# Optimization experiments

Hardware: AMD Instinct MI355X
Metric: run time of the kernel (lower is better)

## Reference

```python
import jax, jax.numpy as jnp
import numpy as np

D_MODEL = 1024
HIDDEN = 2048
D_STATE = 16
KERN = 3
BATCH = 2
SEQ = 2048


def _layernorm(x, g, b, eps=1e-5):
    m = jnp.mean(x, axis=-1, keepdims=True)
    v = jnp.var(x, axis=-1, keepdims=True)
    return (x - m) * jax.lax.rsqrt(v + eps) * g + b


def setup_inputs() -> dict:
    key = jax.random.key(0)
    ks = jax.random.split(key, 10)
    w_scale = 0.02  # keep pre-activations in a sane range (mimics trained-net init)
    return {
        "x": jax.random.normal(ks[0], (BATCH, SEQ, D_MODEL), jnp.float32),
        "W_x": jax.random.normal(ks[1], (HIDDEN, D_MODEL), jnp.float32) * w_scale,
        "b_x": jnp.zeros((HIDDEN,), jnp.float32),
        "W_g": jax.random.normal(ks[2], (HIDDEN, D_MODEL), jnp.float32) * w_scale,
        "b_g": jnp.zeros((HIDDEN,), jnp.float32),
        "conv_w": jax.random.normal(ks[3], (HIDDEN, 1, KERN), jnp.float32) * 0.3,
        "conv_b": jnp.zeros((HIDDEN,), jnp.float32),
        "A_raw": jax.random.normal(ks[4], (HIDDEN, D_STATE), jnp.float32),
        "B_ssm": jax.random.normal(ks[5], (HIDDEN, D_STATE), jnp.float32),
        "C_ssm": jax.random.normal(ks[6], (HIDDEN, D_STATE), jnp.float32),
        "W_dt": jax.random.normal(ks[7], (HIDDEN, D_MODEL), jnp.float32) * w_scale,
        "b_dt": jnp.zeros((HIDDEN,), jnp.float32),
        "W_out": jax.random.normal(ks[8], (D_MODEL, HIDDEN), jnp.float32) * w_scale,
        "b_out": jnp.zeros((D_MODEL,), jnp.float32),
        "ln_g": jnp.ones((D_MODEL,), jnp.float32),
        "ln_b": jnp.zeros((D_MODEL,), jnp.float32),
    }


def reference(x, W_x, b_x, W_g, b_g, conv_w, conv_b, A_raw, B_ssm, C_ssm,
              W_dt, b_dt, W_out, b_out, ln_g, ln_b):
    # projections: u, gate
    u = jnp.einsum('bld,hd->blh', x, W_x) + b_x                    # [B,L,H]
    g = jax.nn.sigmoid(jnp.einsum('bld,hd->blh', x, W_g) + b_g)    # [B,L,H]
    # depthwise conv over time (padding = kernel//2, 'same' for odd kernel)
    pad = conv_w.shape[-1] // 2
    h = jax.lax.conv_general_dilated(
        jnp.transpose(u, (0, 2, 1)), conv_w,
        window_strides=(1,), padding=[(pad, pad)],
        feature_group_count=conv_w.shape[0],
        dimension_numbers=('NCH', 'OIH', 'NCH')) + conv_b[None, :, None]
    h = jnp.transpose(h, (0, 2, 1))                                # [B,L,H]
    u = u * g + h * (1.0 - g)
    # time-invariant dt per channel (mean over batch & time, clamped)
    dt = jax.nn.softplus(jnp.einsum('bld,hd->blh', x, W_dt) + b_dt).mean(axis=(0, 1))
    dt = jnp.clip(dt, 1e-3, 2.0)                                   # [H]
    # discretize
    A = -jax.nn.softplus(A_raw)                                    # [H,S]
    A_d = jnp.exp(A * dt[:, None])                                 # [H,S]
    B_d = (A_d - 1.0) / (A + 1e-6) * B_ssm                         # [H,S]
    # selective scan: state s[b,h,k] = A_d*s + B_d*u_t ; y = <s, C>
    Bsz, L, H = u.shape
    S = A_d.shape[1]

    def step(carry, u_t):                                          # u_t: [B,H]
        new = A_d[None] * carry + B_d[None] * u_t[:, :, None]      # [B,H,S]
        y_t = jnp.einsum('bhs,hs->bh', new, C_ssm)
        return new, y_t

    init = jnp.zeros((Bsz, H, S), dtype=u.dtype)
    _, ys = jax.lax.scan(step, init, jnp.transpose(u, (1, 0, 2)))  # ys: [L,B,H]
    y = jnp.transpose(ys, (1, 0, 2))                               # [B,L,H]
    out = jnp.einsum('blh,dh->bld', y, W_out) + b_out
    return _layernorm(x + out, ln_g, ln_b)
```

## Files before the change

### kernel.cpp

```cpp
#include <hip/hip_runtime.h>
#include <math.h>

#define D_MODEL 1024
#define HIDDEN  2048
#define D_STATE 16
#define BATCH   2
#define SEQ     2048
#define NTOK    (BATCH*SEQ)
#define CHUNK   64
#define NCHUNK  (SEQ/CHUNK)

typedef __attribute__((ext_vector_type(8))) short bf16x8;
typedef __attribute__((ext_vector_type(8))) unsigned short ushort8;
typedef __attribute__((ext_vector_type(4))) float f32x4;

#define GLOAD_LDS16(gptr, lptr) \
    __builtin_amdgcn_global_load_lds((const __attribute__((address_space(1))) void*)(gptr), \
                                     (__attribute__((address_space(3))) void*)(lptr), 16, 0, 0)

__device__ __forceinline__ float softplus_f(float x) {
    return fmaxf(x, 0.0f) + log1pf(expf(-fabsf(x)));
}
__device__ __forceinline__ float sigmoid_f(float x) {
    return 1.0f / (1.0f + expf(-x));
}
__device__ __forceinline__ ushort f2bf(float f) {
    unsigned u = __float_as_uint(f);
    unsigned r = (u + 0x7fffu + ((u >> 16) & 1u)) >> 16;
    return (ushort)r;
}
__device__ __forceinline__ float bf2f(ushort u) {
    return __uint_as_float(((unsigned)u) << 16);
}

__global__ __launch_bounds__(256) void cvt_all(
    const float* __restrict__ x, const float* __restrict__ Wx,
    const float* __restrict__ Wg, const float* __restrict__ Wdt,
    const float* __restrict__ Wout, ushort* __restrict__ arena)
{
    int i = blockIdx.x * 256 + threadIdx.x;
    const float* src; int base;
    if      (i < 1048576) { src = x;    base = 0; }
    else if (i < 1572864) { src = Wx;   base = 1048576; }
    else if (i < 2097152) { src = Wg;   base = 1572864; }
    else if (i < 2621440) { src = Wdt;  base = 2097152; }
    else                  { src = Wout; base = 2621440; }
    float4 v = reinterpret_cast<const float4*>(src)[i - base];
    ushort4 o = { f2bf(v.x), f2bf(v.y), f2bf(v.z), f2bf(v.w) };
    reinterpret_cast<ushort4*>(arena)[i] = o;
}

__device__ __forceinline__ void kloop_pipe1024(
    const ushort* __restrict__ A, const ushort* __restrict__ B,
    int ldA, int ldB, ushort* As, ushort* Bs,
    f32x4 (&acc)[4][4], int lane, int w, int wm, int wn)
{
    const int lr   = lane >> 2;
    const int kc   = (lane & 3) * 8;
    const int quad = lane >> 4;
    const int fr   = lane & 15;

    const int slab0 = w * 2;
    const int r0 = slab0 * 16 + lr;
    const int r1 = r0 + 16;
    const ushort* pa0 = A + (size_t)r0 * ldA + kc;
    const ushort* pa1 = A + (size_t)r1 * ldA + kc;
    const ushort* pb0 = B + (size_t)r0 * ldB + kc;
    const ushort* pb1 = B + (size_t)r1 * ldB + kc;

    GLOAD_LDS16(pa0,      &As[slab0 * 512]);
    GLOAD_LDS16(pa1,      &As[slab0 * 512 + 512]);
    GLOAD_LDS16(pb0,      &Bs[slab0 * 512]);
    GLOAD_LDS16(pb1,      &Bs[slab0 * 512 + 512]);
    GLOAD_LDS16(pa0 + 32, &As[4096 + slab0 * 512]);
    GLOAD_LDS16(pa1 + 32, &As[4096 + slab0 * 512 + 512]);
    GLOAD_LDS16(pb0 + 32, &Bs[4096 + slab0 * 512]);
    GLOAD_LDS16(pb1 + 32, &Bs[4096 + slab0 * 512 + 512]);

    #pragma unroll
    for (int i = 0; i < 32; i++) {
        if (i == 31) { asm volatile("s_waitcnt vmcnt(0) lgkmcnt(0)" ::: "memory"); }
        else         { asm volatile("s_waitcnt vmcnt(4) lgkmcnt(0)" ::: "memory"); }
        asm volatile("s_barrier" ::: "memory");
        if (i + 2 < 32) {
            const int nb = (i + 2) % 3;
            GLOAD_LDS16(pa0 + (i + 2) * 32, &As[nb * 4096 + slab0 * 512]);
            GLOAD_LDS16(pa1 + (i + 2) * 32, &As[nb * 4096 + slab0 * 512 + 512]);
            GLOAD_LDS16(pb0 + (i + 2) * 32, &Bs[nb * 4096 + slab0 * 512]);
            GLOAD_LDS16(pb1 + (i + 2) * 32, &Bs[nb * 4096 + slab0 * 512 + 512]);
        }
        const int buf = i % 3;
        const ushort* as = &As[buf * 4096];
        const ushort* bs = &Bs[buf * 4096];
        bf16x8 af[4], bfv[4];
        #pragma unroll
        for (int t = 0; t < 4; t++) {
            af[t]  = *reinterpret_cast<const bf16x8*>(&as[(wm * 64 + t * 16 + fr) * 32 + quad * 8]);
            bfv[t] = *reinterpret_cast<const bf16x8*>(&bs[(wn * 64 + t * 16 + fr) * 32 + quad * 8]);
        }
        #pragma unroll
        for (int ii = 0; ii < 4; ii++)
            #pragma unroll
            for (int jj = 0; jj < 4; jj++)
                acc[ii][jj] = __builtin_amdgcn_mfma_f32_16x16x32_bf16(af[ii], bfv[jj], acc[ii][jj], 0, 0, 0);
    }
    asm volatile("s_waitcnt vmcnt(0) lgkmcnt(0)" ::: "memory");
    asm volatile("s_barrier" ::: "memory");
}

__global__ __launch_bounds__(256) void proj_gemm_fused(
    const ushort* __restrict__ xbf, const ushort* __restrict__ Wcat,
    const float* __restrict__ b_x, const float* __restrict__ b_g,
    const float* __restrict__ b_dt, ushort* __restrict__ u_out,
    ushort* __restrict__ g_out, float* __restrict__ dt_sum)
{
    __shared__ ushort S[24576];
    ushort* As = S;
    ushort* Bs = S + 12288;
    const int tid = threadIdx.x, lane = tid & 63, w = tid >> 6;
    const int wm = w & 1, wn = w >> 1;
    const int m0 = blockIdx.x * 128, n0 = blockIdx.y * 128;
    const int quad = lane >> 4, fr = lane & 15;

    f32x4 acc[4][4];
    #pragma unroll
    for (int i = 0; i < 4; i++)
        #pragma unroll
        for (int j = 0; j < 4; j++)
            acc[i][j] = (f32x4){0.f, 0.f, 0.f, 0.f};

    kloop_pipe1024(xbf + (size_t)m0 * D_MODEL, Wcat + (size_t)n0 * D_MODEL,
                   D_MODEL, D_MODEL, As, Bs, acc, lane, w, wm, wn);

    const int region = n0 >> 11;
    const int ncb = n0 & 2047;

    if (region == 2) {
        #pragma unroll
        for (int j = 0; j < 4; j++) {
            int n = ncb + wn * 64 + j * 16 + fr;
            float bj = b_dt[n];
            float s = 0.f;
            #pragma unroll
            for (int i = 0; i < 4; i++)
                #pragma unroll
                for (int r = 0; r < 4; r++)
                    s += softplus_f(acc[i][j][r] + bj);
            s += __shfl_xor(s, 16);
            s += __shfl_xor(s, 32);
            if (lane < 16) atomicAdd(&dt_sum[n], s);
        }
    } else {
        const float* bias = region ? b_g : b_x;
        ushort* out = region ? g_out : u_out;
        ushort* Cs = S;
        #pragma unroll
        for (int j = 0; j < 4; j++) {
            int col = wn * 64 + j * 16 + fr;
            float bj = bias[ncb + col];
            #pragma unroll
            for (int i = 0; i < 4; i++) {
                int row = wm * 64 + i * 16 + quad * 4;
                #pragma unroll
                for (int r = 0; r < 4; r++) {
                    float v = acc[i][j][r] + bj;
                    if (region) v = sigmoid_f(v);
                    Cs[(row + r) * 128 + col] = f2bf(v);
                }
            }
        }
        __syncthreads();
        #pragma unroll
        for (int k = 0; k < 8; k++) {
            int v = k * 256 + tid;
            int row = v >> 4, c = (v & 15) * 8;
            *reinterpret_cast<ushort8*>(&out[(size_t)(m0 + row) * HIDDEN + ncb + c]) =
                *reinterpret_cast<const ushort8*>(&Cs[v * 8]);
        }
    }
}

__global__ __launch_bounds__(256) void gemm_out(
    const ushort* __restrict__ ybf, const ushort* __restrict__ Wout,
    float* __restrict__ p0, float* __restrict__ p1)
{
    __shared__ ushort S[24576];
    ushort* As = S;
    ushort* Bs = S + 12288;
    const int tid = threadIdx.x, lane = tid & 63, w = tid >> 6;
    const int wm = w & 1, wn = w >> 1;
    const int m0 = blockIdx.x * 128;
    const int nt = blockIdx.y >> 1, ks = blockIdx.y & 1;
    const int n0 = nt * 128;
    const int quad = lane >> 4, fr = lane & 15;

    f32x4 acc[4][4];
    #pragma unroll
    for (int i = 0; i < 4; i++)
        #pragma unroll
        for (int j = 0; j < 4; j++)
            acc[i][j] = (f32x4){0.f, 0.f, 0.f, 0.f};

    kloop_pipe1024(ybf + (size_t)m0 * HIDDEN + ks * 1024,
                   Wout + (size_t)n0 * HIDDEN + ks * 1024,
                   HIDDEN, HIDDEN, As, Bs, acc, lane, w, wm, wn);

    float* pk = ks ? p1 : p0;
    float* Sf = (float*)S;
    #pragma unroll
    for (int phase = 0; phase < 2; phase++) {
        if (wm == phase) {
            #pragma unroll
            for (int j = 0; j < 4; j++) {
                int col = wn * 64 + j * 16 + fr;
                #pragma unroll
                for (int i = 0; i < 4; i++) {
                    int row = i * 16 + quad * 4;
                    #pragma unroll
                    for (int r = 0; r < 4; r++)
                        Sf[(row + r) * 128 + col] = acc[i][j][r];
                }
            }
        }
        __syncthreads();
        #pragma unroll
        for (int k = 0; k < 8; k++) {
            int v = k * 256 + tid;
            int row = v >> 5, c = (v & 31) * 4;
            size_t off = (size_t)(m0 + phase * 64 + row) * D_MODEL + n0 + c;
            *reinterpret_cast<float4*>(&pk[off]) =
                *reinterpret_cast<const float4*>(&Sf[v * 4]);
        }
        __syncthreads();
    }
}

__global__ __launch_bounds__(256) void dt_finalize(
    const float* __restrict__ dt_sum, const float* __restrict__ A_raw,
    const float* __restrict__ B_ssm, float* __restrict__ A_d,
    float* __restrict__ B_d, float* __restrict__ A_dL)
{
    int i = blockIdx.x * 256 + threadIdx.x;
    if (i >= HIDDEN * D_STATE) return;
    int h = i >> 4;
    float dt = dt_sum[h] * (1.0f / NTOK);
    dt = fminf(fmaxf(dt, 1e-3f), 2.0f);
    float Av = -softplus_f(A_raw[i]);
    float Ad = expf(Av * dt);
    float Bd = (Ad - 1.0f) / (Av + 1e-6f) * B_ssm[i];
    A_d[i] = Ad;
    B_d[i] = Bd;
    A_dL[i] = expf(Av * dt * CHUNK);
}

__global__ __launch_bounds__(256) void scan_pass1(
    const ushort* __restrict__ u_bf, const ushort* __restrict__ g_bf,
    const float* __restrict__ conv_w, const float* __restrict__ conv_b,
    const float* __restrict__ A_d, const float* __restrict__ B_d,
    const float* __restrict__ C_ssm,
    ushort* __restrict__ ypart, float* __restrict__ states)
{
    int idx = blockIdx.x * 256 + threadIdx.x;
    int h  = idx & (HIDDEN - 1);
    int bc = idx >> 11;
    int c  = bc & (NCHUNK - 1);
    int b  = bc >> 5;
    float Ad[D_STATE], Bd[D_STATE], Cv[D_STATE], st[D_STATE];
    const float4* a4 = reinterpret_cast<const float4*>(A_d  + h * D_STATE);
    const float4* b4 = reinterpret_cast<const float4*>(B_d  + h * D_STATE);
    const float4* c4 = reinterpret_cast<const float4*>(C_ssm + h * D_STATE);
    #pragma unroll
    for (int q = 0; q < 4; q++) {
        float4 av = a4[q], bv = b4[q], cv = c4[q];
        Ad[q*4+0]=av.x; Ad[q*4+1]=av.y; Ad[q*4+2]=av.z; Ad[q*4+3]=av.w;
        Bd[q*4+0]=bv.x; Bd[q*4+1]=bv.y; Bd[q*4+2]=bv.z; Bd[q*4+3]=bv.w;
        Cv[q*4+0]=cv.x; Cv[q*4+1]=cv.y; Cv[q*4+2]=cv.z; Cv[q*4+3]=cv.w;
    }
    #pragma unroll
    for (int s = 0; s < D_STATE; s++) st[s] = 0.f;

    float w0 = conv_w[h * 3 + 0], w1 = conv_w[h * 3 + 1];
    float w2 = conv_w[h * 3 + 2], cb = conv_b[h];
    const int tok0 = c * CHUNK;
    const size_t base = ((size_t)b * SEQ + tok0) * HIDDEN + h;
    float u_prev = (tok0 > 0) ? bf2f(u_bf[base - HIDDEN]) : 0.f;
    float u_cur  = bf2f(u_bf[base]);
    for (int l = 0; l < CHUNK; l++) {
        float u_next = (tok0 + l + 1 < SEQ) ? bf2f(u_bf[base + (size_t)(l + 1) * HIDDEN]) : 0.f;
        float gv = bf2f(g_bf[base + (size_t)l * HIDDEN]);
        float conv = u_prev * w0 + u_cur * w1 + u_next * w2 + cb;
        float uv = u_cur * gv + conv * (1.0f - gv);
        float y0 = 0.f, y1 = 0.f, y2 = 0.f, y3 = 0.f;
        #pragma unroll
        for (int s = 0; s < D_STATE; s += 4) {
            st[s+0] = fmaf(Ad[s+0], st[s+0], Bd[s+0] * uv);
            st[s+1] = fmaf(Ad[s+1], st[s+1], Bd[s+1] * uv);
            st[s+2] = fmaf(Ad[s+2], st[s+2], Bd[s+2] * uv);
            st[s+3] = fmaf(Ad[s+3], st[s+3], Bd[s+3] * uv);
            y0 = fmaf(st[s+0], Cv[s+0], y0);
            y1 = fmaf(st[s+1], Cv[s+1], y1);
            y2 = fmaf(st[s+2], Cv[s+2], y2);
            y3 = fmaf(st[s+3], Cv[s+3], y3);
        }
        ypart[base + (size_t)l * HIDDEN] = f2bf((y0 + y1) + (y2 + y3));
        u_prev = u_cur; u_cur = u_next;
    }
    float4* sp = reinterpret_cast<float4*>(states + ((size_t)bc * HIDDEN + h) * D_STATE);
    #pragma unroll
    for (int q = 0; q < 4; q++)
        sp[q] = (float4){st[q*4+0], st[q*4+1], st[q*4+2], st[q*4+3]};
}

__global__ __launch_bounds__(256) void scan_pass2(
    float* __restrict__ states, const float* __restrict__ A_dL)
{
    int idx = blockIdx.x * 256 + threadIdx.x;
    int s = idx & 15;
    int h = (idx >> 4) & (HIDDEN - 1);
    int b = idx >> 15;
    float aL = A_dL[h * D_STATE + s];
    float carry = 0.f;
    for (int c = 0; c < NCHUNK; c++) {
        size_t addr = (((size_t)(b * NCHUNK + c) * HIDDEN) + h) * D_STATE + s;
        float fin = states[addr];
        states[addr] = carry;
        carry = fmaf(aL, carry, fin);
    }
}

__global__ __launch_bounds__(256) void scan_pass3(
    const ushort* __restrict__ ypart, const float* __restrict__ states,
    const float* __restrict__ A_d, const float* __restrict__ C_ssm,
    ushort* __restrict__ ybf)
{
    int idx = blockIdx.x * 256 + threadIdx.x;
    int h  = idx & (HIDDEN - 1);
    int bc = idx >> 11;
    int c  = bc & (NCHUNK - 1);
    int b  = bc >> 5;
    float Ad[D_STATE], t[D_STATE];
    const float* sp = states + ((size_t)bc * HIDDEN + h) * D_STATE;
    #pragma unroll
    for (int s = 0; s < D_STATE; s++) {
        float a = A_d[h * D_STATE + s];
        Ad[s] = a;
        t[s] = C_ssm[h * D_STATE + s] * a * sp[s];
    }
    const size_t base = ((size_t)b * SEQ + (size_t)c * CHUNK) * HIDDEN + h;
    for (int l = 0; l < CHUNK; l++) {
        float c0 = 0.f, c1 = 0.f;
        #pragma unroll
        for (int s = 0; s < D_STATE; s += 2) {
            c0 += t[s];
            c1 += t[s + 1];
            t[s] *= Ad[s];
            t[s + 1] *= Ad[s + 1];
        }
        ybf[base + (size_t)l * HIDDEN] = f2bf(bf2f(ypart[base + (size_t)l * HIDDEN]) + (c0 + c1));
    }
}

__global__ __launch_bounds__(256) void ln_kernel(
    const float* __restrict__ x, const float* __restrict__ p0,
    const float* __restrict__ p1, const float* __restrict__ b_out,
    const float* __restrict__ ln_g, const float* __restrict__ ln_b,
    float* __restrict__ out)
{
    int row = blockIdx.x;
    int tid = threadIdx.x;
    const float4 xv = reinterpret_cast<const float4*>(x  + (size_t)row * D_MODEL)[tid];
    const float4 a0 = reinterpret_cast<const float4*>(p0 + (size_t)row * D_MODEL)[tid];
    const float4 a1 = reinterpret_cast<const float4*>(p1 + (size_t)row * D_MODEL)[tid];
    const float4 bo = reinterpret_cast<const float4*>(b_out)[tid];
    float4 v;
    v.x = xv.x + bo.x + a0.x + a1.x;
    v.y = xv.y + bo.y + a0.y + a1.y;
    v.z = xv.z + bo.z + a0.z + a1.z;
    v.w = xv.w + bo.w + a0.w + a1.w;
    float s  = v.x + v.y + v.z + v.w;
    float ss = v.x * v.x + v.y * v.y + v.z * v.z + v.w * v.w;
    #pragma unroll
    for (int off = 32; off > 0; off >>= 1) {
        s  += __shfl_down(s, off);
        ss += __shfl_down(ss, off);
    }
    __shared__ float sbuf[4], ssbuf[4];
    int wid = tid >> 6, lane = tid & 63;
    if (lane == 0) { sbuf[wid] = s; ssbuf[wid] = ss; }
    __syncthreads();
    float tot  = sbuf[0] + sbuf[1] + sbuf[2] + sbuf[3];
    float tot2 = ssbuf[0] + ssbuf[1] + ssbuf[2] + ssbuf[3];
    float mean = tot * (1.0f / D_MODEL);
    float var  = tot2 * (1.0f / D_MODEL) - mean * mean;
    float rstd = rsqrtf(var + 1e-5f);
    const float4 gv = reinterpret_cast<const float4*>(ln_g)[tid];
    const float4 bv = reinterpret_cast<const float4*>(ln_b)[tid];
    float4 o;
    o.x = (v.x - mean) * rstd * gv.x + bv.x;
    o.y = (v.y - mean) * rstd * gv.y + bv.y;
    o.z = (v.z - mean) * rstd * gv.z + bv.z;
    o.w = (v.w - mean) * rstd * gv.w + bv.w;
    reinterpret_cast<float4*>(out + (size_t)row * D_MODEL)[tid] = o;
}

extern "C" void kernel_launch(void* const* d_in, const int* in_sizes, int n_in,
                              void* d_out, int out_size, void* d_ws, size_t ws_size,
                              hipStream_t stream) {
    const float* x      = (const float*)d_in[0];
    const float* W_x    = (const float*)d_in[1];
    const float* b_x    = (const float*)d_in[2];
    const float* W_g    = (const float*)d_in[3];
    const float* b_g    = (const float*)d_in[4];
    const float* conv_w = (const float*)d_in[5];
    const float* conv_b = (const float*)d_in[6];
    const float* A_raw  = (const float*)d_in[7];
    const float* B_ssm  = (const float*)d_in[8];
    const float* C_ssm  = (const float*)d_in[9];
    const float* W_dt   = (const float*)d_in[10];
    const float* b_dt   = (const float*)d_in[11];
    const float* W_out  = (const float*)d_in[12];
    const float* b_out  = (const float*)d_in[13];
    const float* ln_g   = (const float*)d_in[14];
    const float* ln_b   = (const float*)d_in[15];

    char* W = (char*)d_ws;
    ushort* arena   = (ushort*)(W);
    ushort* x_bf    = arena;
    ushort* Wcat    = arena + 4194304;
    ushort* Wout_bf = arena + 10485760;
    ushort* u_bf    = (ushort*)(W + (24ull << 20));
    ushort* g_bf    = (ushort*)(W + (40ull << 20));
    ushort* ypart   = (ushort*)(W + (56ull << 20));
    float*  states  = (float*)(W + (72ull << 20));
    float*  dt_sum  = (float*)(W + (80ull << 20));
    float*  A_d     = (float*)(W + (80ull << 20) + 65536);
    float*  B_d     = (float*)(W + (80ull << 20) + 65536 + 131072);
    float*  A_dL    = (float*)(W + (80ull << 20) + 65536 + 262144);
    ushort* y_bf    = u_bf;
    float*  p0      = (float*)g_bf;
    float*  p1      = (float*)ypart;

    hipMemsetAsync(dt_sum, 0, HIDDEN * sizeof(float), stream);

    dim3 blk(256);
    cvt_all<<<12288, blk, 0, stream>>>(x, W_x, W_g, W_dt, W_out, arena);

    dim3 grid_proj(NTOK / 128, 3 * HIDDEN / 128);
    proj_gemm_fused<<<grid_proj, blk, 0, stream>>>(x_bf, Wcat, b_x, b_g, b_dt,
                                                   u_bf, g_bf, dt_sum);
    dt_finalize<<<(HIDDEN * D_STATE) / 256, blk, 0, stream>>>(dt_sum, A_raw, B_ssm,
                                                              A_d, B_d, A_dL);
    scan_pass1<<<(BATCH * NCHUNK * HIDDEN) / 256, blk, 0, stream>>>(
        u_bf, g_bf, conv_w, conv_b, A_d, B_d, C_ssm, ypart, states);
    scan_pass2<<<(BATCH * HIDDEN * D_STATE) / 256, blk, 0, stream>>>(states, A_dL);
    scan_pass3<<<(BATCH * NCHUNK * HIDDEN) / 256, blk, 0, stream>>>(ypart, states, A_d,
                                                                    C_ssm, y_bf);
    dim3 grid_out(NTOK / 128, (D_MODEL / 128) * 2);
    gemm_out<<<grid_out, blk, 0, stream>>>(y_bf, Wout_bf, p0, p1);
    ln_kernel<<<NTOK, blk, 0, stream>>>(x, p0, p1, b_out, ln_g, ln_b, (float*)d_out);
}
```

Before: 295.8 us.

## Fuse dt finalize and three scan passes into one cooperative kernel

Merges dt_finalize, scan_pass1, scan_pass2 and scan_pass3 into a single cooperative kernel that uses grid-wide syncs between phases. The dt_sum memset moves into the conversion kernel. This is meant to remove several kernel launches and the gaps between them, and it lets the scan keep A_d, C and the indices in registers across phases. In exchange it adds grid sync cost. The grid is 512 blocks of 256 threads, and all of them must be co-resident; pass2 also runs only 64K threads, so half the grid sits idle in that phase.

```diff
diff --git a/kernel.cpp b/kernel.cpp
--- a/kernel.cpp
+++ b/kernel.cpp
@@ -1,4 +1,5 @@
 #include <hip/hip_runtime.h>
+#include <hip/hip_cooperative_groups.h>
 #include <math.h>
 
 #define D_MODEL 1024
@@ -36,9 +37,11 @@
 __global__ __launch_bounds__(256) void cvt_all(
     const float* __restrict__ x, const float* __restrict__ Wx,
     const float* __restrict__ Wg, const float* __restrict__ Wdt,
-    const float* __restrict__ Wout, ushort* __restrict__ arena)
+    const float* __restrict__ Wout, ushort* __restrict__ arena,
+    float* __restrict__ dt_sum)
 {
     int i = blockIdx.x * 256 + threadIdx.x;
+    if (i < 512) reinterpret_cast<float4*>(dt_sum)[i] = (float4){0.f, 0.f, 0.f, 0.f};
     const float* src; int base;
     if      (i < 1048576) { src = x;    base = 0; }
     else if (i < 1572864) { src = Wx;   base = 1048576; }
@@ -235,128 +238,115 @@
     }
 }
 
-__global__ __launch_bounds__(256) void dt_finalize(
-    const float* __restrict__ dt_sum, const float* __restrict__ A_raw,
-    const float* __restrict__ B_ssm, float* __restrict__ A_d,
-    float* __restrict__ B_d, float* __restrict__ A_dL)
-{
-    int i = blockIdx.x * 256 + threadIdx.x;
-    if (i >= HIDDEN * D_STATE) return;
-    int h = i >> 4;
-    float dt = dt_sum[h] * (1.0f / NTOK);
-    dt = fminf(fmaxf(dt, 1e-3f), 2.0f);
-    float Av = -softplus_f(A_raw[i]);
-    float Ad = expf(Av * dt);
-    float Bd = (Ad - 1.0f) / (Av + 1e-6f) * B_ssm[i];
-    A_d[i] = Ad;
-    B_d[i] = Bd;
-    A_dL[i] = expf(Av * dt * CHUNK);
-}
-
-__global__ __launch_bounds__(256) void scan_pass1(
+__global__ __launch_bounds__(256) void scan_fused(
     const ushort* __restrict__ u_bf, const ushort* __restrict__ g_bf,
     const float* __restrict__ conv_w, const float* __restrict__ conv_b,
-    const float* __restrict__ A_d, const float* __restrict__ B_d,
-    const float* __restrict__ C_ssm,
-    ushort* __restrict__ ypart, float* __restrict__ states)
-{
-    int idx = blockIdx.x * 256 + threadIdx.x;
-    int h  = idx & (HIDDEN - 1);
-    int bc = idx >> 11;
-    int c  = bc & (NCHUNK - 1);
-    int b  = bc >> 5;
+    const float* __restrict__ dt_sum, const float* __restrict__ A_raw,
+    const float* __restrict__ B_ssm, const float* __restrict__ C_ssm,
+    ushort* __restrict__ ypart, float* __restrict__ states,
+    float* __restrict__ A_dg, float* __restrict__ B_dg,
+    float* __restrict__ A_dL, ushort* __restrict__ ybf)
+{
+    cooperative_groups::grid_group gg = cooperative_groups::this_grid();
+    const int idx = blockIdx.x * 256 + threadIdx.x;
+
+    if (idx < HIDDEN * D_STATE) {
+        int h0 = idx >> 4;
+        float dt = fminf(fmaxf(dt_sum[h0] * (1.0f / NTOK), 1e-3f), 2.0f);
+        float Av = -softplus_f(A_raw[idx]);
+        float a = expf(Av * dt);
+        A_dg[idx] = a;
+        B_dg[idx] = (a - 1.0f) / (Av + 1e-6f) * B_ssm[idx];
+        A_dL[idx] = expf(Av * dt * CHUNK);
+    }
+    gg.sync();
+
+    const int h  = idx & (HIDDEN - 1);
+    const int bc = idx >> 11;
+    const int c  = bc & (NCHUNK - 1);
+    const int b  = bc >> 5;
     float Ad[D_STATE], Bd[D_STATE], Cv[D_STATE], st[D_STATE];
-    const float4* a4 = reinterpret_cast<const float4*>(A_d  + h * D_STATE);
-    const float4* b4 = reinterpret_cast<const float4*>(B_d  + h * D_STATE);
-    const float4* c4 = reinterpret_cast<const float4*>(C_ssm + h * D_STATE);
-    #pragma unroll
-    for (int q = 0; q < 4; q++) {
-        float4 av = a4[q], bv = b4[q], cv = c4[q];
-        Ad[q*4+0]=av.x; Ad[q*4+1]=av.y; Ad[q*4+2]=av.z; Ad[q*4+3]=av.w;
-        Bd[q*4+0]=bv.x; Bd[q*4+1]=bv.y; Bd[q*4+2]=bv.z; Bd[q*4+3]=bv.w;
-        Cv[q*4+0]=cv.x; Cv[q*4+1]=cv.y; Cv[q*4+2]=cv.z; Cv[q*4+3]=cv.w;
+    {
+        const float4* a4 = reinterpret_cast<const float4*>(A_dg + h * D_STATE);
+        const float4* b4 = reinterpret_cast<const float4*>(B_dg + h * D_STATE);
+        const float4* c4 = reinterpret_cast<const float4*>(C_ssm + h * D_STATE);
+        #pragma unroll
+        for (int q = 0; q < 4; q++) {
+            float4 av = a4[q], bv = b4[q], cv = c4[q];
+            Ad[q*4+0]=av.x; Ad[q*4+1]=av.y; Ad[q*4+2]=av.z; Ad[q*4+3]=av.w;
+            Bd[q*4+0]=bv.x; Bd[q*4+1]=bv.y; Bd[q*4+2]=bv.z; Bd[q*4+3]=bv.w;
+            Cv[q*4+0]=cv.x; Cv[q*4+1]=cv.y; Cv[q*4+2]=cv.z; Cv[q*4+3]=cv.w;
+        }
     }
     #pragma unroll
     for (int s = 0; s < D_STATE; s++) st[s] = 0.f;
 
-    float w0 = conv_w[h * 3 + 0], w1 = conv_w[h * 3 + 1];
-    float w2 = conv_w[h * 3 + 2], cb = conv_b[h];
+    const float w0 = conv_w[h * 3 + 0], w1 = conv_w[h * 3 + 1];
+    const float w2 = conv_w[h * 3 + 2], cb = conv_b[h];
     const int tok0 = c * CHUNK;
     const size_t base = ((size_t)b * SEQ + tok0) * HIDDEN + h;
-    float u_prev = (tok0 > 0) ? bf2f(u_bf[base - HIDDEN]) : 0.f;
-    float u_cur  = bf2f(u_bf[base]);
-    for (int l = 0; l < CHUNK; l++) {
-        float u_next = (tok0 + l + 1 < SEQ) ? bf2f(u_bf[base + (size_t)(l + 1) * HIDDEN]) : 0.f;
-        float gv = bf2f(g_bf[base + (size_t)l * HIDDEN]);
-        float conv = u_prev * w0 + u_cur * w1 + u_next * w2 + cb;
-        float uv = u_cur * gv + conv * (1.0f - gv);
-        float y0 = 0.f, y1 = 0.f, y2 = 0.f, y3 = 0.f;
-        #pragma unroll
-        for (int s = 0; s < D_STATE; s += 4) {
-            st[s+0] = fmaf(Ad[s+0], st[s+0], Bd[s+0] * uv);
-            st[s+1] = fmaf(Ad[s+1], st[s+1], Bd[s+1] * uv);
-            st[s+2] = fmaf(Ad[s+2], st[s+2], Bd[s+2] * uv);
-            st[s+3] = fmaf(Ad[s+3], st[s+3], Bd[s+3] * uv);
-            y0 = fmaf(st[s+0], Cv[s+0], y0);
-            y1 = fmaf(st[s+1], Cv[s+1], y1);
-            y2 = fmaf(st[s+2], Cv[s+2], y2);
-            y3 = fmaf(st[s+3], Cv[s+3], y3);
-        }
-        ypart[base + (size_t)l * HIDDEN] = f2bf((y0 + y1) + (y2 + y3));
-        u_prev = u_cur; u_cur = u_next;
-    }
-    float4* sp = reinterpret_cast<float4*>(states + ((size_t)bc * HIDDEN + h) * D_STATE);
-    #pragma unroll
-    for (int q = 0; q < 4; q++)
-        sp[q] = (float4){st[q*4+0], st[q*4+1], st[q*4+2], st[q*4+3]};
-}
-
-__global__ __launch_bounds__(256) void scan_pass2(
-    float* __restrict__ states, const float* __restrict__ A_dL)
-{
-    int idx = blockIdx.x * 256 + threadIdx.x;
-    int s = idx & 15;
-    int h = (idx >> 4) & (HIDDEN - 1);
-    int b = idx >> 15;
-    float aL = A_dL[h * D_STATE + s];
-    float carry = 0.f;
-    for (int c = 0; c < NCHUNK; c++) {
-        size_t addr = (((size_t)(b * NCHUNK + c) * HIDDEN) + h) * D_STATE + s;
-        float fin = states[addr];
-        states[addr] = carry;
-        carry = fmaf(aL, carry, fin);
-    }
-}
-
-__global__ __launch_bounds__(256) void scan_pass3(
-    const ushort* __restrict__ ypart, const float* __restrict__ states,
-    const float* __restrict__ A_d, const float* __restrict__ C_ssm,
-    ushort* __restrict__ ybf)
-{
-    int idx = blockIdx.x * 256 + threadIdx.x;
-    int h  = idx & (HIDDEN - 1);
-    int bc = idx >> 11;
-    int c  = bc & (NCHUNK - 1);
-    int b  = bc >> 5;
-    float Ad[D_STATE], t[D_STATE];
-    const float* sp = states + ((size_t)bc * HIDDEN + h) * D_STATE;
-    #pragma unroll
-    for (int s = 0; s < D_STATE; s++) {
-        float a = A_d[h * D_STATE + s];
-        Ad[s] = a;
-        t[s] = C_ssm[h * D_STATE + s] * a * sp[s];
-    }
-    const size_t base = ((size_t)b * SEQ + (size_t)c * CHUNK) * HIDDEN + h;
-    for (int l = 0; l < CHUNK; l++) {
-        float c0 = 0.f, c1 = 0.f;
-        #pragma unroll
-        for (int s = 0; s < D_STATE; s += 2) {
-            c0 += t[s];
-            c1 += t[s + 1];
-            t[s] *= Ad[s];
-            t[s + 1] *= Ad[s + 1];
-        }
-        ybf[base + (size_t)l * HIDDEN] = f2bf(bf2f(ypart[base + (size_t)l * HIDDEN]) + (c0 + c1));
+    {
+        float u_prev = (tok0 > 0) ? bf2f(u_bf[base - HIDDEN]) : 0.f;
+        float u_cur  = bf2f(u_bf[base]);
+        for (int l = 0; l < CHUNK; l++) {
+            float u_next = (tok0 + l + 1 < SEQ) ? bf2f(u_bf[base + (size_t)(l + 1) * HIDDEN]) : 0.f;
+            float gv = bf2f(g_bf[base + (size_t)l * HIDDEN]);
+            float conv = u_prev * w0 + u_cur * w1 + u_next * w2 + cb;
+            float uv = u_cur * gv + conv * (1.0f - gv);
+            float y0 = 0.f, y1 = 0.f, y2 = 0.f, y3 = 0.f;
+            #pragma unroll
+            for (int s = 0; s < D_STATE; s += 4) {
+                st[s+0] = fmaf(Ad[s+0], st[s+0], Bd[s+0] * uv);
+                st[s+1] = fmaf(Ad[s+1], st[s+1], Bd[s+1] * uv);
+                st[s+2] = fmaf(Ad[s+2], st[s+2], Bd[s+2] * uv);
+                st[s+3] = fmaf(Ad[s+3], st[s+3], Bd[s+3] * uv);
+                y0 = fmaf(st[s+0], Cv[s+0], y0);
+                y1 = fmaf(st[s+1], Cv[s+1], y1);
+                y2 = fmaf(st[s+2], Cv[s+2], y2);
+                y3 = fmaf(st[s+3], Cv[s+3], y3);
+            }
+            ypart[base + (size_t)l * HIDDEN] = f2bf((y0 + y1) + (y2 + y3));
+            u_prev = u_cur; u_cur = u_next;
+        }
+        float4* sp = reinterpret_cast<float4*>(states + ((size_t)bc * HIDDEN + h) * D_STATE);
+        #pragma unroll
+        for (int q = 0; q < 4; q++)
+            sp[q] = (float4){st[q*4+0], st[q*4+1], st[q*4+2], st[q*4+3]};
+    }
+    gg.sync();
+
+    if (idx < BATCH * HIDDEN * D_STATE) {
+        int s2 = idx & 15;
+        int h2 = (idx >> 4) & (HIDDEN - 1);
+        int b2 = idx >> 15;
+        float aL = A_dL[h2 * D_STATE + s2];
+        float carry = 0.f;
+        for (int cc = 0; cc < NCHUNK; cc++) {
+            size_t addr = (((size_t)(b2 * NCHUNK + cc) * HIDDEN) + h2) * D_STATE + s2;
+            float fin = states[addr];
+            states[addr] = carry;
+            carry = fmaf(aL, carry, fin);
+        }
+    }
+    gg.sync();
+
+    {
+        float t[D_STATE];
+        const float* sp = states + ((size_t)bc * HIDDEN + h) * D_STATE;
+        #pragma unroll
+        for (int s = 0; s < D_STATE; s++)
+            t[s] = Cv[s] * Ad[s] * sp[s];
+        for (int l = 0; l < CHUNK; l++) {
+            float c0 = 0.f, c1 = 0.f;
+            #pragma unroll
+            for (int s = 0; s < D_STATE; s += 2) {
+                c0 += t[s];
+                c1 += t[s + 1];
+                t[s] *= Ad[s];
+                t[s + 1] *= Ad[s + 1];
+            }
+            ybf[base + (size_t)l * HIDDEN] = f2bf(bf2f(ypart[base + (size_t)l * HIDDEN]) + (c0 + c1));
+        }
     }
 }
 
@@ -440,21 +430,22 @@
     float*  p0      = (float*)g_bf;
     float*  p1      = (float*)ypart;
 
-    hipMemsetAsync(dt_sum, 0, HIDDEN * sizeof(float), stream);
-
     dim3 blk(256);
-    cvt_all<<<12288, blk, 0, stream>>>(x, W_x, W_g, W_dt, W_out, arena);
+    cvt_all<<<12288, blk, 0, stream>>>(x, W_x, W_g, W_dt, W_out, arena, dt_sum);
 
     dim3 grid_proj(NTOK / 128, 3 * HIDDEN / 128);
     proj_gemm_fused<<<grid_proj, blk, 0, stream>>>(x_bf, Wcat, b_x, b_g, b_dt,
                                                    u_bf, g_bf, dt_sum);
-    dt_finalize<<<(HIDDEN * D_STATE) / 256, blk, 0, stream>>>(dt_sum, A_raw, B_ssm,
-                                                              A_d, B_d, A_dL);
-    scan_pass1<<<(BATCH * NCHUNK * HIDDEN) / 256, blk, 0, stream>>>(
-        u_bf, g_bf, conv_w, conv_b, A_d, B_d, C_ssm, ypart, states);
-    scan_pass2<<<(BATCH * HIDDEN * D_STATE) / 256, blk, 0, stream>>>(states, A_dL);
-    scan_pass3<<<(BATCH * NCHUNK * HIDDEN) / 256, blk, 0, stream>>>(ypart, states, A_d,
-                                                                    C_ssm, y_bf);
+
+    {
+        void* args[] = { (void*)&u_bf, (void*)&g_bf, (void*)&conv_w, (void*)&conv_b,
+                         (void*)&dt_sum, (void*)&A_raw, (void*)&B_ssm, (void*)&C_ssm,
+                         (void*)&ypart, (void*)&states, (void*)&A_d, (void*)&B_d,
+                         (void*)&A_dL, (void*)&y_bf };
+        hipLaunchCooperativeKernel((void*)scan_fused, dim3(512), dim3(256),
+                                   args, 0, stream);
+    }
+
     dim3 grid_out(NTOK / 128, (D_MODEL / 128) * 2);
     gemm_out<<<grid_out, blk, 0, stream>>>(y_bf, Wout_bf, p0, p1);
     ln_kernel<<<NTOK, blk, 0, stream>>>(x, p0, p1, b_out, ln_g, ln_b, (float*)d_out);
```

Measured after the change: 486.4 us. 64.5% more time.
